# Performance work log

Measured on AMD Instinct MI355X. Metric: run time of the kernel, lower is better.

Reference implementation:

```python
import jax, jax.numpy as jnp
import numpy as np

NUM_HEADS = 16
HEAD_DIM = 128


def rotate_half(x):
    x1, x2 = jnp.split(x, 2, axis=-1)
    return jnp.concatenate((-x2, x1), axis=-1)


def setup_inputs() -> dict:
    key = jax.random.key(0)
    ks = jax.random.split(key, 6)
    B, S, H = 2, 2048, 2048
    hidden_states = jax.random.normal(ks[0], (B, S, H), dtype=jnp.float32)
    # RoPE cos/sin tables (HF-style: half-dim freqs duplicated)
    inv_freq = 1.0 / (10000.0 ** (jnp.arange(0, HEAD_DIM, 2, dtype=jnp.float32) / HEAD_DIM))
    t = jnp.arange(S, dtype=jnp.float32)
    freqs = jnp.outer(t, inv_freq)                      # [S, HEAD_DIM/2]
    emb = jnp.concatenate((freqs, freqs), axis=-1)      # [S, HEAD_DIM]
    cos = jnp.cos(emb)
    sin = jnp.sin(emb)
    attention_mask = jnp.zeros((1, 1, S, S), dtype=jnp.float32)
    scale = 0.02
    Wq = jax.random.normal(ks[1], (H, H), dtype=jnp.float32) * scale
    Wk = jax.random.normal(ks[2], (H, H), dtype=jnp.float32) * scale
    Wv = jax.random.normal(ks[3], (H, H), dtype=jnp.float32) * scale
    Wo = jax.random.normal(ks[4], (H, H), dtype=jnp.float32) * scale
    return {"hidden_states": hidden_states, "cos": cos, "sin": sin,
            "attention_mask": attention_mask, "Wq": Wq, "Wk": Wk, "Wv": Wv, "Wo": Wo}


def reference(hidden_states, cos, sin, attention_mask, Wq, Wk, Wv, Wo):
    B, S, H = hidden_states.shape
    nh, hd = NUM_HEADS, HEAD_DIM
    # nn.Linear(bias=False): x @ W.T
    q = hidden_states @ Wq.T
    k = hidden_states @ Wk.T
    v = hidden_states @ Wv.T
    # [B, nh, S, hd]
    q = q.reshape(B, S, nh, hd).transpose(0, 2, 1, 3)
    k = k.reshape(B, S, nh, hd).transpose(0, 2, 1, 3)
    v = v.reshape(B, S, nh, hd).transpose(0, 2, 1, 3)
    # RoPE
    c = cos[None, None, :, :]
    s = sin[None, None, :, :]
    q = q * c + rotate_half(q) * s
    k = k * c + rotate_half(k) * s
    scores = jnp.einsum("bhqd,bhkd->bhqk", q, k) / jnp.sqrt(jnp.float32(hd))
    scores = scores + attention_mask
    attn = jax.nn.softmax(scores, axis=-1)
    out = jnp.einsum("bhqk,bhkd->bhqd", attn, v)
    out = out.transpose(0, 2, 1, 3).reshape(B, S, H)
    return out @ Wo.T
```

## Files before the change

kernel.cpp:

```cpp
#include <hip/hip_runtime.h>
#include <stdint.h>

typedef __bf16 bf16;
typedef __attribute__((ext_vector_type(4))) __bf16 bf16x4;
typedef __attribute__((ext_vector_type(8))) __bf16 bf16x8;
typedef __attribute__((ext_vector_type(4))) float f32x4;
typedef __attribute__((ext_vector_type(4))) short short4v;

__device__ __forceinline__ void gl2lds16(const void* g, void* l) {
  __builtin_amdgcn_global_load_lds(
      (__attribute__((address_space(1))) void*)(uintptr_t)g,
      (__attribute__((address_space(3))) void*)(uint32_t)(uintptr_t)l,
      16, 0, 0);
}

__device__ __forceinline__ f32x4 mfma_16x16x16(bf16x4 a, bf16x4 b, f32x4 c) {
#if defined(__HIP_DEVICE_COMPILE__)
  return __builtin_amdgcn_mfma_f32_16x16x16bf16_1k(
      __builtin_bit_cast(short4v, a), __builtin_bit_cast(short4v, b), c, 0, 0, 0);
#else
  return c;
#endif
}

__global__ __launch_bounds__(256) void cast_to_bf16(const float* __restrict__ x,
                                                    bf16* __restrict__ y, int n4) {
  int i = blockIdx.x * 256 + threadIdx.x;
  if (i >= n4) return;
  float4 v = ((const float4*)x)[i];
  bf16x4 o;
  o[0] = (bf16)v.x; o[1] = (bf16)v.y; o[2] = (bf16)v.z; o[3] = (bf16)v.w;
  ((bf16x4*)y)[i] = o;
}

__global__ __launch_bounds__(256) void cast_w4(const float* __restrict__ s0,
                                               const float* __restrict__ s1,
                                               const float* __restrict__ s2,
                                               const float* __restrict__ s3,
                                               bf16* __restrict__ d0, bf16* __restrict__ d1,
                                               bf16* __restrict__ d2, bf16* __restrict__ d3) {
  int i = blockIdx.x * 256 + threadIdx.x;
  int wsel = i >> 20;
  int j = i & 1048575;
  const float* s = wsel == 0 ? s0 : wsel == 1 ? s1 : wsel == 2 ? s2 : s3;
  bf16* d = wsel == 0 ? d0 : wsel == 1 ? d1 : wsel == 2 ? d2 : d3;
  float4 v = ((const float4*)s)[j];
  bf16x4 o;
  o[0] = (bf16)v.x; o[1] = (bf16)v.y; o[2] = (bf16)v.z; o[3] = (bf16)v.w;
  ((bf16x4*)d)[j] = o;
}

template <int BM, int BN, typename OutT>
__global__ __launch_bounds__(512) void gemm_t(const bf16* __restrict__ A,
                                              const bf16* __restrict__ B,
                                              OutT* __restrict__ C,
                                              int M, int N, int K) {
  constexpr int WGM = 2, WGN = 4;
  constexpr int FM = BM / WGM / 16;
  constexpr int FN = BN / WGN / 16;
  constexpr int NPH = FM / 2;
  constexpr int CH_A = BM / 8;
  constexpr int CH_TOT = (BM + BN) / 8;
  constexpr int CHW = CH_TOT / 8;

  __shared__ bf16 As[3][BM * 64];
  __shared__ bf16 Bs[3][BN * 64];

  const int t = threadIdx.x;
  const int w = t >> 6;
  const int lane = t & 63;
  const int quad = lane >> 4;
  const int m16 = lane & 15;
  const int wr = w / WGN;
  const int wc = w % WGN;
  const size_t rowA0 = (size_t)blockIdx.y * BM;
  const size_t rowB0 = (size_t)blockIdx.x * BN;

  f32x4 acc[FM][FN];
#pragma unroll
  for (int i = 0; i < FM; ++i)
#pragma unroll
    for (int j = 0; j < FN; ++j) { f32x4 z = {0.f, 0.f, 0.f, 0.f}; acc[i][j] = z; }

  const int srow = lane >> 3;
  const int sg = (lane & 7) ^ (srow & 7);

  auto stage1 = [&](int buf, int kt, int j) {
    const int g = w * CHW + j;
    if (g < CH_A) {
      gl2lds16(A + (rowA0 + g * 8 + srow) * (size_t)K + kt * 64 + sg * 8,
               &As[buf][g * 512]);
    } else {
      const int gb = g - CH_A;
      gl2lds16(B + (rowB0 + gb * 8 + srow) * (size_t)K + kt * 64 + sg * 8,
               &Bs[buf][gb * 512]);
    }
  };

  auto read_af = [&](bf16x8 (&af)[2][2], int c, int p) {
#pragma unroll
    for (int mi = 0; mi < 2; ++mi)
#pragma unroll
      for (int ks = 0; ks < 2; ++ks)
        af[mi][ks] = *(const bf16x8*)&As[c][((wr * FM + p * 2 + mi) * 16 + m16) * 64 +
                                            (((ks * 4 + quad) ^ (m16 & 7)) * 8)];
  };

  const int NT = K >> 6;
#pragma unroll
  for (int j = 0; j < CHW; ++j) stage1(0, 0, j);
#pragma unroll
  for (int j = 0; j < CHW; ++j) stage1(1, 1, j);
  asm volatile("s_waitcnt vmcnt(6)" ::: "memory");
  __builtin_amdgcn_s_barrier();

  int c0 = 0, c2 = 2;
#pragma unroll 1
  for (int kt = 0; kt < NT; ++kt) {
    if (kt + 2 < NT) {
#pragma unroll
      for (int j = 0; j < CHW; ++j) stage1(c2, kt + 2, j);
    }

    bf16x8 bfr[FN][2];
#pragma unroll
    for (int fn = 0; fn < FN; ++fn)
#pragma unroll
      for (int ks = 0; ks < 2; ++ks)
        bfr[fn][ks] = *(const bf16x8*)&Bs[c0][((wc * FN + fn) * 16 + m16) * 64 +
                                              (((ks * 4 + quad) ^ (m16 & 7)) * 8)];
    bf16x8 afp[2][2][2];
    read_af(afp[0], c0, 0);

#pragma unroll
    for (int p = 0; p < NPH; ++p) {
      const int pb = p & 1;
      if (p + 1 < NPH) read_af(afp[pb ^ 1], c0, p + 1);
      __builtin_amdgcn_s_barrier();
      __builtin_amdgcn_s_setprio(1);
#pragma unroll
      for (int ks = 0; ks < 2; ++ks)
#pragma unroll
        for (int mi = 0; mi < 2; ++mi)
#pragma unroll
          for (int fn = 0; fn < FN; ++fn)
            acc[p * 2 + mi][fn] = __builtin_amdgcn_mfma_f32_16x16x32_bf16(
                afp[pb][mi][ks], bfr[fn][ks], acc[p * 2 + mi][fn], 0, 0, 0);
      __builtin_amdgcn_s_setprio(0);
      if (p + 1 < NPH) __builtin_amdgcn_s_barrier();
    }
    if (kt < NT - 3) asm volatile("s_waitcnt vmcnt(6)" ::: "memory");
    else             asm volatile("s_waitcnt vmcnt(0)" ::: "memory");
    __builtin_amdgcn_s_barrier();
    c0 = (c0 == 2) ? 0 : c0 + 1;
    c2 = (c2 == 2) ? 0 : c2 + 1;
  }

#pragma unroll
  for (int fm = 0; fm < FM; ++fm)
#pragma unroll
    for (int fn = 0; fn < FN; ++fn)
#pragma unroll
      for (int r = 0; r < 4; ++r) {
        size_t row = rowA0 + (wr * FM + fm) * 16 + quad * 4 + r;
        size_t col = rowB0 + (wc * FN + fn) * 16 + m16;
        float v = acc[fm][fn][r];
        if constexpr (__is_same(OutT, float)) C[row * N + col] = v;
        else                                  C[row * N + col] = (bf16)v;
      }
}

__global__ __launch_bounds__(256) void rope_kernel(bf16* __restrict__ X,
                                                   const float* __restrict__ cosp,
                                                   const float* __restrict__ sinp) {
  int tid = blockIdx.x * 256 + threadIdx.x;
  int g = tid & 7;
  int hh = (tid >> 3) & 31;
  int tok = tid >> 8;
  int s = tok & 2047;
  const float sl2e = 0.088388347648318447f * 1.4426950408889634f;
  float qs = hh < 16 ? sl2e : 1.0f;
  size_t base = (size_t)tok * 4096 + hh * 128 + g * 8;
  bf16x8 x1 = *(const bf16x8*)&X[base];
  bf16x8 x2 = *(const bf16x8*)&X[base + 64];
  float4 c0 = *(const float4*)&cosp[s * 128 + g * 8];
  float4 c1 = *(const float4*)&cosp[s * 128 + g * 8 + 4];
  float4 s0 = *(const float4*)&sinp[s * 128 + g * 8];
  float4 s1 = *(const float4*)&sinp[s * 128 + g * 8 + 4];
  float cc[8] = {c0.x, c0.y, c0.z, c0.w, c1.x, c1.y, c1.z, c1.w};
  float ss[8] = {s0.x, s0.y, s0.z, s0.w, s1.x, s1.y, s1.z, s1.w};
  bf16x8 o1, o2;
#pragma unroll
  for (int j = 0; j < 8; ++j) {
    float a = (float)x1[j], b = (float)x2[j];
    o1[j] = (bf16)((a * cc[j] - b * ss[j]) * qs);
    o2[j] = (bf16)((b * cc[j] + a * ss[j]) * qs);
  }
  *(bf16x8*)&X[base]      = o1;
  *(bf16x8*)&X[base + 64] = o2;
}

__global__ __launch_bounds__(256) void flash_attn(const bf16* __restrict__ Qg,
                                                  const bf16* __restrict__ Kg,
                                                  const bf16* __restrict__ Vt,
                                                  bf16* __restrict__ O) {
  __shared__ bf16 Ks[2][64 * 128];
  __shared__ bf16 Vs[2][128 * 64];

  const int t = threadIdx.x;
  const int w = t >> 6;
  const int lane = t & 63;
  const int quad = lane >> 4;
  const int m16 = lane & 15;
  const int qt = blockIdx.x;
  const int bh = blockIdx.y;
  const int b = bh >> 4;
  const int h = bh & 15;

  bf16x8 qf[2][4];
#pragma unroll
  for (int half = 0; half < 2; ++half) {
    const int qrow = qt * 128 + w * 32 + half * 16 + m16;
    const bf16* qp = Qg + (size_t)(b * 2048 + qrow) * 4096 + h * 128 + quad * 8;
#pragma unroll
    for (int ks = 0; ks < 4; ++ks) qf[half][ks] = *(const bf16x8*)(qp + ks * 32);
  }

  const int krl = lane >> 4;
  const int vrl = lane >> 3;
  const int vg = (lane & 7) ^ (vrl & 7);

  auto stage = [&](int buf, int kt) {
#pragma unroll
    for (int i = 0; i < 4; ++i) {
      const int c = w * 4 + i;
      const int krow = c * 4 + krl;
      const int kgg = (lane & 15) ^ (krow & 15);
      gl2lds16(Kg + (size_t)(b * 2048 + kt * 64 + krow) * 4096 + h * 128 + kgg * 8,
               &Ks[buf][c * 512]);
      const int vrow = c * 8 + vrl;
      gl2lds16(Vt + (size_t)(h * 128 + vrow) * 4096 + b * 2048 + kt * 64 + vg * 8,
               &Vs[buf][c * 512]);
    }
  };

  f32x4 o[2][8];
#pragma unroll
  for (int half = 0; half < 2; ++half)
#pragma unroll
    for (int i = 0; i < 8; ++i) { f32x4 z = {0.f, 0.f, 0.f, 0.f}; o[half][i] = z; }
  float lsum[2] = {0.f, 0.f};

  stage(0, 0);

#pragma unroll 1
  for (int kt = 0; kt < 32; ++kt) {
    const int cur = kt & 1;
    __syncthreads();
    if (kt < 31) stage(cur ^ 1, kt + 1);

    f32x4 st[2][4];
#pragma unroll
    for (int half = 0; half < 2; ++half)
#pragma unroll
      for (int nb = 0; nb < 4; ++nb) {
        f32x4 z = {0.f, 0.f, 0.f, 0.f};
        st[half][nb] = z;
      }
    __builtin_amdgcn_s_setprio(1);
#pragma unroll
    for (int ks = 0; ks < 4; ++ks)
#pragma unroll
      for (int nb = 0; nb < 4; ++nb) {
        bf16x8 kf = *(const bf16x8*)&Ks[cur][(nb * 16 + m16) * 128 + ((ks * 4 + quad) ^ m16) * 8];
        st[0][nb] = __builtin_amdgcn_mfma_f32_16x16x32_bf16(kf, qf[0][ks], st[0][nb], 0, 0, 0);
        st[1][nb] = __builtin_amdgcn_mfma_f32_16x16x32_bf16(kf, qf[1][ks], st[1][nb], 0, 0, 0);
      }
    __builtin_amdgcn_s_setprio(0);

    bf16x4 pA[2][4];
#pragma unroll
    for (int half = 0; half < 2; ++half)
#pragma unroll
      for (int nb = 0; nb < 4; ++nb)
#pragma unroll
        for (int r = 0; r < 4; ++r) {
          float p = __builtin_amdgcn_exp2f(st[half][nb][r]);
          lsum[half] += p;
          pA[half][nb][r] = (bf16)p;
        }

    __builtin_amdgcn_s_setprio(1);
#pragma unroll
    for (int nb = 0; nb < 4; ++nb)
#pragma unroll
      for (int db = 0; db < 8; ++db) {
        bf16x4 vB = *(const bf16x4*)&Vs[cur][(db * 16 + m16) * 64 +
            (((nb * 2 + (quad >> 1)) ^ (m16 & 7)) * 8 + (quad & 1) * 4)];
        o[0][db] = mfma_16x16x16(vB, pA[0][nb], o[0][db]);
        o[1][db] = mfma_16x16x16(vB, pA[1][nb], o[1][db]);
      }
    __builtin_amdgcn_s_setprio(0);
  }

#pragma unroll
  for (int half = 0; half < 2; ++half) {
    lsum[half] += __shfl_xor(lsum[half], 16);
    lsum[half] += __shfl_xor(lsum[half], 32);
  }
  float inv[2] = {1.0f / lsum[0], 1.0f / lsum[1]};

#pragma unroll
  for (int half = 0; half < 2; ++half) {
    const int row = qt * 128 + w * 32 + half * 16 + m16;
    bf16* op = O + (size_t)(b * 2048 + row) * 2048 + h * 128 + quad * 4;
#pragma unroll
    for (int db = 0; db < 8; ++db) {
      bf16x4 ov;
#pragma unroll
      for (int r = 0; r < 4; ++r) ov[r] = (bf16)(o[half][db][r] * inv[half]);
      *(bf16x4*)(op + db * 16) = ov;
    }
  }
}

extern "C" void kernel_launch(void* const* d_in, const int* in_sizes, int n_in,
                              void* d_out, int out_size, void* d_ws, size_t ws_size,
                              hipStream_t stream) {
  const float* hs   = (const float*)d_in[0];
  const float* cosp = (const float*)d_in[1];
  const float* sinp = (const float*)d_in[2];
  const float* Wq   = (const float*)d_in[4];
  const float* Wk   = (const float*)d_in[5];
  const float* Wv   = (const float*)d_in[6];
  const float* Wo   = (const float*)d_in[7];
  float* out = (float*)d_out;

  char* ws = (char*)d_ws;
  bf16* Xb   = (bf16*)(ws);
  bf16* Wqkb = (bf16*)(ws + 16777216);
  bf16* Wvb  = (bf16*)(ws + 33554432);
  bf16* Wob  = (bf16*)(ws + 41943040);
  bf16* QKb  = (bf16*)(ws + 50331648);
  bf16* Vtb  = (bf16*)(ws + 83886080);
  bf16* Ob   = Xb;

  cast_to_bf16<<<8192, 256, 0, stream>>>(hs, Xb, 2097152);
  cast_w4<<<16384, 256, 0, stream>>>(Wq, Wk, Wv, Wo,
                                     Wqkb, Wqkb + 4194304, Wvb, Wob);

  gemm_t<128, 256, bf16><<<dim3(16, 32), 512, 0, stream>>>(
      Xb, Wqkb, QKb, 4096, 4096, 2048);
  gemm_t<128, 256, bf16><<<dim3(16, 16), 512, 0, stream>>>(
      Wvb, Xb, Vtb, 2048, 4096, 2048);

  rope_kernel<<<4096, 256, 0, stream>>>(QKb, cosp, sinp);

  flash_attn<<<dim3(16, 32), 256, 0, stream>>>(QKb, QKb + 2048, Vtb, Ob);

  gemm_t<128, 256, float><<<dim3(8, 32), 512, 0, stream>>>(
      Ob, Wob, out, 4096, 2048, 2048);
}
```

Measured before the change: 406.7 us.

## Retile GEMMs, double-buffer GEMM pipeline, load V directly to registers in attention

The GEMM kernel drops from a 3-stage to a 2-stage LDS pipeline with full vmcnt(0) waits, and gains a configurable warp grid. Tile shapes change: QK projection uses 256x256 tiles, and the output projection uses 256x128 with a 4x2 warp grid. Flash attention stops staging V through LDS and instead reads V fragments from global memory into registers each iteration. It also adds an occupancy hint of 2 blocks per SM. The aim is to cut LDS footprint and traffic and raise occupancy, at the cost of less latency hiding in the GEMMs and uncoalesced V reads exposed in the attention loop.

```diff
diff --git a/kernel.cpp b/kernel.cpp
--- a/kernel.cpp
+++ b/kernel.cpp
@@ -50,12 +50,11 @@
   ((bf16x4*)d)[j] = o;
 }
 
-template <int BM, int BN, typename OutT>
+template <int BM, int BN, int WGM, int WGN, typename OutT>
 __global__ __launch_bounds__(512) void gemm_t(const bf16* __restrict__ A,
                                               const bf16* __restrict__ B,
                                               OutT* __restrict__ C,
                                               int M, int N, int K) {
-  constexpr int WGM = 2, WGN = 4;
   constexpr int FM = BM / WGM / 16;
   constexpr int FN = BN / WGN / 16;
   constexpr int NPH = FM / 2;
@@ -63,8 +62,8 @@
   constexpr int CH_TOT = (BM + BN) / 8;
   constexpr int CHW = CH_TOT / 8;
 
-  __shared__ bf16 As[3][BM * 64];
-  __shared__ bf16 Bs[3][BN * 64];
+  __shared__ bf16 As[2][BM * 64];
+  __shared__ bf16 Bs[2][BN * 64];
 
   const int t = threadIdx.x;
   const int w = t >> 6;
@@ -106,20 +105,18 @@
                                             (((ks * 4 + quad) ^ (m16 & 7)) * 8)];
   };
 
+#pragma unroll
+  for (int j = 0; j < CHW; ++j) stage1(0, 0, j);
+  asm volatile("s_waitcnt vmcnt(0)" ::: "memory");
+  __builtin_amdgcn_s_barrier();
+
   const int NT = K >> 6;
-#pragma unroll
-  for (int j = 0; j < CHW; ++j) stage1(0, 0, j);
-#pragma unroll
-  for (int j = 0; j < CHW; ++j) stage1(1, 1, j);
-  asm volatile("s_waitcnt vmcnt(6)" ::: "memory");
-  __builtin_amdgcn_s_barrier();
-
-  int c0 = 0, c2 = 2;
 #pragma unroll 1
   for (int kt = 0; kt < NT; ++kt) {
-    if (kt + 2 < NT) {
-#pragma unroll
-      for (int j = 0; j < CHW; ++j) stage1(c2, kt + 2, j);
+    const int c = kt & 1;
+    if (kt + 1 < NT) {
+#pragma unroll
+      for (int j = 0; j < CHW; ++j) stage1(c ^ 1, kt + 1, j);
     }
 
     bf16x8 bfr[FN][2];
@@ -127,15 +124,15 @@
     for (int fn = 0; fn < FN; ++fn)
 #pragma unroll
       for (int ks = 0; ks < 2; ++ks)
-        bfr[fn][ks] = *(const bf16x8*)&Bs[c0][((wc * FN + fn) * 16 + m16) * 64 +
-                                              (((ks * 4 + quad) ^ (m16 & 7)) * 8)];
+        bfr[fn][ks] = *(const bf16x8*)&Bs[c][((wc * FN + fn) * 16 + m16) * 64 +
+                                             (((ks * 4 + quad) ^ (m16 & 7)) * 8)];
     bf16x8 afp[2][2][2];
-    read_af(afp[0], c0, 0);
+    read_af(afp[0], c, 0);
 
 #pragma unroll
     for (int p = 0; p < NPH; ++p) {
       const int pb = p & 1;
-      if (p + 1 < NPH) read_af(afp[pb ^ 1], c0, p + 1);
+      if (p + 1 < NPH) read_af(afp[pb ^ 1], c, p + 1);
       __builtin_amdgcn_s_barrier();
       __builtin_amdgcn_s_setprio(1);
 #pragma unroll
@@ -149,11 +146,8 @@
       __builtin_amdgcn_s_setprio(0);
       if (p + 1 < NPH) __builtin_amdgcn_s_barrier();
     }
-    if (kt < NT - 3) asm volatile("s_waitcnt vmcnt(6)" ::: "memory");
-    else             asm volatile("s_waitcnt vmcnt(0)" ::: "memory");
+    asm volatile("s_waitcnt vmcnt(0)" ::: "memory");
     __builtin_amdgcn_s_barrier();
-    c0 = (c0 == 2) ? 0 : c0 + 1;
-    c2 = (c2 == 2) ? 0 : c2 + 1;
   }
 
 #pragma unroll
@@ -200,12 +194,11 @@
   *(bf16x8*)&X[base + 64] = o2;
 }
 
-__global__ __launch_bounds__(256) void flash_attn(const bf16* __restrict__ Qg,
-                                                  const bf16* __restrict__ Kg,
-                                                  const bf16* __restrict__ Vt,
-                                                  bf16* __restrict__ O) {
+__global__ __launch_bounds__(256, 2) void flash_attn(const bf16* __restrict__ Qg,
+                                                     const bf16* __restrict__ Kg,
+                                                     const bf16* __restrict__ Vt,
+                                                     bf16* __restrict__ O) {
   __shared__ bf16 Ks[2][64 * 128];
-  __shared__ bf16 Vs[2][128 * 64];
 
   const int t = threadIdx.x;
   const int w = t >> 6;
@@ -227,8 +220,6 @@
   }
 
   const int krl = lane >> 4;
-  const int vrl = lane >> 3;
-  const int vg = (lane & 7) ^ (vrl & 7);
 
   auto stage = [&](int buf, int kt) {
 #pragma unroll
@@ -238,11 +229,10 @@
       const int kgg = (lane & 15) ^ (krow & 15);
       gl2lds16(Kg + (size_t)(b * 2048 + kt * 64 + krow) * 4096 + h * 128 + kgg * 8,
                &Ks[buf][c * 512]);
-      const int vrow = c * 8 + vrl;
-      gl2lds16(Vt + (size_t)(h * 128 + vrow) * 4096 + b * 2048 + kt * 64 + vg * 8,
-               &Vs[buf][c * 512]);
     }
   };
+
+  const bf16* Vb = Vt + (size_t)(h * 128 + m16) * 4096 + b * 2048 + quad * 4;
 
   f32x4 o[2][8];
 #pragma unroll
@@ -257,6 +247,14 @@
   for (int kt = 0; kt < 32; ++kt) {
     const int cur = kt & 1;
     __syncthreads();
+
+    bf16x4 vr[8][4];
+#pragma unroll
+    for (int db = 0; db < 8; ++db)
+#pragma unroll
+      for (int nb = 0; nb < 4; ++nb)
+        vr[db][nb] = *(const bf16x4*)(Vb + ((size_t)db * 65536 + kt * 64 + nb * 16));
+
     if (kt < 31) stage(cur ^ 1, kt + 1);
 
     f32x4 st[2][4];
@@ -295,10 +293,8 @@
     for (int nb = 0; nb < 4; ++nb)
 #pragma unroll
       for (int db = 0; db < 8; ++db) {
-        bf16x4 vB = *(const bf16x4*)&Vs[cur][(db * 16 + m16) * 64 +
-            (((nb * 2 + (quad >> 1)) ^ (m16 & 7)) * 8 + (quad & 1) * 4)];
-        o[0][db] = mfma_16x16x16(vB, pA[0][nb], o[0][db]);
-        o[1][db] = mfma_16x16x16(vB, pA[1][nb], o[1][db]);
+        o[0][db] = mfma_16x16x16(vr[db][nb], pA[0][nb], o[0][db]);
+        o[1][db] = mfma_16x16x16(vr[db][nb], pA[1][nb], o[1][db]);
       }
     __builtin_amdgcn_s_setprio(0);
   }
@@ -349,15 +345,15 @@
   cast_w4<<<16384, 256, 0, stream>>>(Wq, Wk, Wv, Wo,
                                      Wqkb, Wqkb + 4194304, Wvb, Wob);
 
-  gemm_t<128, 256, bf16><<<dim3(16, 32), 512, 0, stream>>>(
+  gemm_t<256, 256, 2, 4, bf16><<<dim3(16, 16), 512, 0, stream>>>(
       Xb, Wqkb, QKb, 4096, 4096, 2048);
-  gemm_t<128, 256, bf16><<<dim3(16, 16), 512, 0, stream>>>(
+  gemm_t<128, 256, 2, 4, bf16><<<dim3(16, 16), 512, 0, stream>>>(
       Wvb, Xb, Vtb, 2048, 4096, 2048);
 
   rope_kernel<<<4096, 256, 0, stream>>>(QKb, cosp, sinp);
 
   flash_attn<<<dim3(16, 32), 256, 0, stream>>>(QKb, QKb + 2048, Vtb, Ob);
 
-  gemm_t<128, 256, float><<<dim3(8, 32), 512, 0, stream>>>(
+  gemm_t<256, 128, 4, 2, float><<<dim3(16, 16), 512, 0, stream>>>(
       Ob, Wob, out, 4096, 2048, 2048);
 }
```

Result: slower. 564.3 us (+38.7%).
